# Performance work log

Hardware: AMD Instinct MI355X
Metric: run time of the kernel (lower is better)

## Reference

```python
import jax, jax.numpy as jnp
import numpy as np

D, H, O, E, N = 1024, 2048, 1024, 8, 4096

def setup_inputs() -> dict:
    key = jax.random.key(0)
    ks = jax.random.split(key, 5)
    scale = lambda fan_in: 1.0 / np.sqrt(fan_in)
    x = jax.random.normal(ks[0], (N, D), dtype=jnp.float32)
    Wr = jax.random.normal(ks[1], (E, D), dtype=jnp.float32) * scale(D)
    br = jnp.zeros((E,), dtype=jnp.float32)
    W1 = jax.random.normal(ks[2], (E, H, D), dtype=jnp.float32) * scale(D)
    b1 = jnp.zeros((E, H), dtype=jnp.float32)
    W2 = jax.random.normal(ks[3], (E, O, H), dtype=jnp.float32) * scale(H)
    b2 = jnp.zeros((E, O), dtype=jnp.float32)
    return {"x": x, "Wr": Wr, "br": br, "W1": W1, "b1": b1, "W2": W2, "b2": b2}

def reference(x, Wr, br, W1, b1, W2, b2):
    # router softmax over experts: [N, E]
    route = jax.nn.softmax(x @ Wr.T + br, axis=-1)
    # all experts as one grouped GEMM: hidden [N, E, H]
    h = jnp.einsum('nd,ehd->neh', x, W1) + b1
    h = jnp.square(jax.nn.relu(h))  # squared ReLU
    # expert outputs [N, E, O]
    y = jnp.einsum('neh,eoh->neo', h, W2) + b2
    # softmax-weighted combine over experts -> [N, O]
    return jnp.einsum('ne,neo->no', route, y)
```

## Files before the change

kernel.cpp:

```cpp
#include <hip/hip_runtime.h>
#include <hip/hip_bf16.h>
#include <stdint.h>

#define Dd 1024
#define Hd 2048
#define Od 1024
#define Ed 8
#define Nd 4096

typedef __bf16 bf16x8 __attribute__((ext_vector_type(8)));
typedef float f32x4 __attribute__((ext_vector_type(4)));

__device__ __forceinline__ void gload16(const void* g, void* l) {
  __builtin_amdgcn_global_load_lds(
      (const __attribute__((address_space(1))) void*)g,
      (__attribute__((address_space(3))) void*)l, 16, 0, 0);
}

__device__ __forceinline__ unsigned short f2bf(float f) {
  __hip_bfloat16 h = __float2bfloat16(f);
  return *reinterpret_cast<unsigned short*>(&h);
}

__global__ void cvt_kernel(const float* __restrict__ in,
                           unsigned short* __restrict__ out, int ngroups) {
  int stride = gridDim.x * blockDim.x;
  for (int g = blockIdx.x * blockDim.x + threadIdx.x; g < ngroups; g += stride) {
    const float4* p = (const float4*)(in + (size_t)g * 8);
    float4 a = p[0], b = p[1];
    unsigned short o[8];
    o[0] = f2bf(a.x); o[1] = f2bf(a.y); o[2] = f2bf(a.z); o[3] = f2bf(a.w);
    o[4] = f2bf(b.x); o[5] = f2bf(b.y); o[6] = f2bf(b.z); o[7] = f2bf(b.w);
    *(int4*)(out + (size_t)g * 8) = *(int4*)o;
  }
}

__global__ void router_kernel(const float* __restrict__ x, const float* __restrict__ Wr,
                              const float* __restrict__ br, float* __restrict__ route,
                              unsigned short* __restrict__ xb) {
  const int n = blockIdx.x;
  const int t = threadIdx.x;
  __shared__ float xs[Dd];
  float4 v = *(const float4*)&x[(size_t)n * Dd + t * 4];
  *(float4*)&xs[t * 4] = v;
  unsigned short o[4] = {f2bf(v.x), f2bf(v.y), f2bf(v.z), f2bf(v.w)};
  *(uint2*)&xb[(size_t)n * Dd + t * 4] = *(const uint2*)o;
  __syncthreads();
  float p[Ed];
  #pragma unroll
  for (int e = 0; e < Ed; ++e) p[e] = 0.f;
  for (int d = t; d < Dd; d += 256) {
    float xv = xs[d];
    #pragma unroll
    for (int e = 0; e < Ed; ++e) p[e] += xv * Wr[e * Dd + d];
  }
  __shared__ float red[Ed][4];
  const int lane = t & 63, wid = t >> 6;
  #pragma unroll
  for (int e = 0; e < Ed; ++e) {
    float vv = p[e];
    for (int off = 32; off > 0; off >>= 1) vv += __shfl_down(vv, off);
    if (lane == 0) red[e][wid] = vv;
  }
  __syncthreads();
  if (t == 0) {
    float lg[Ed], mx = -1e30f;
    #pragma unroll
    for (int e = 0; e < Ed; ++e) {
      lg[e] = red[e][0] + red[e][1] + red[e][2] + red[e][3] + br[e];
      mx = fmaxf(mx, lg[e]);
    }
    float s = 0.f;
    #pragma unroll
    for (int e = 0; e < Ed; ++e) { lg[e] = expf(lg[e] - mx); s += lg[e]; }
    float inv = 1.f / s;
    #pragma unroll
    for (int e = 0; e < Ed; ++e) route[(size_t)n * Ed + e] = lg[e] * inv;
  }
}

__global__ void init_out_kernel(const float* __restrict__ route, const float* __restrict__ b2,
                                float* __restrict__ out) {
  const int idx = blockIdx.x * 256 + threadIdx.x;
  const int n = idx >> 10, o = idx & (Od - 1);
  float s = 0.f;
  #pragma unroll
  for (int e = 0; e < Ed; ++e) s += route[(size_t)n * Ed + e] * b2[e * Od + o];
  out[idx] = s;
}

template <int MODE>
__global__ __launch_bounds__(512, 2) void gemm8p(
    const unsigned short* __restrict__ Ag,
    const unsigned short* __restrict__ Bg,
    const float* __restrict__ bias,
    const float* __restrict__ route,
    void* __restrict__ Cout,
    int n0, int ncRows, int ngx) {
  extern __shared__ unsigned short smem[];
  unsigned short* As = smem;
  unsigned short* Bs = smem + 32768;

  const int nwg = gridDim.x;
  const int orig = blockIdx.x;
  const int q8 = nwg >> 3;
  const int wg = (orig & 7) * q8 + (orig >> 3);
  const int bx = wg % ngx;
  const int rem = wg / ngx;
  int by, ez;
  if (MODE == 0) { by = rem & 7; ez = rem >> 3; }
  else           { by = rem & 3; ez = rem >> 2; }

  const int tid = threadIdx.x;
  const int wid = tid >> 6, lane = tid & 63;
  const int wm = wid >> 2, wn = wid & 3;

  const int trow = tid >> 3;
  const int tcs = ((tid & 7) ^ (trow & 7)) * 8;

  const int NT = (MODE == 0) ? (Dd / 64) : (2 * Hd / 64);

  auto stageA = [&](int buf, int kt, int mh) {
    #pragma unroll
    for (int s = 0; s < 2; ++s) {
      const int pa = mh * 128 + s * 64 + trow;
      const int m = ((pa >> 6) & 1) * 128 + ((pa >> 7) & 1) * 64 + (pa & 63);
      const unsigned short* g;
      if (MODE == 0) {
        g = Ag + (size_t)(n0 + bx * 256 + m) * Dd + kt * 64 + tcs;
      } else {
        const int e = ez * 2 + (kt >> 5);
        g = Ag + (size_t)e * ncRows * Hd + (size_t)(bx * 256 + m) * Hd + (kt & 31) * 64 + tcs;
      }
      gload16(g, &As[(size_t)buf * 16384 + (size_t)(mh * 128 + s * 64) * 64 + wid * 512]);
    }
  };
  auto stageB = [&](int buf, int kt, int nh) {
    #pragma unroll
    for (int s = 0; s < 2; ++s) {
      const int pb = nh * 128 + s * 64 + trow;
      const int n = ((pb >> 5) & 3) * 64 + ((pb >> 7) & 1) * 32 + (pb & 31);
      const unsigned short* g;
      if (MODE == 0) {
        g = Bg + (size_t)ez * Hd * Dd + (size_t)(by * 256 + n) * Dd + kt * 64 + tcs;
      } else {
        const int e = ez * 2 + (kt >> 5);
        g = Bg + (size_t)e * Od * Hd + (size_t)(by * 256 + n) * Hd + (kt & 31) * 64 + tcs;
      }
      gload16(g, &Bs[(size_t)buf * 16384 + (size_t)(nh * 128 + s * 64) * 64 + wid * 512]);
    }
  };

  const int laneRow = lane & 15;
  const int swzc[2] = { ((lane >> 4) ^ (lane & 7)) << 3,
                        (((lane >> 4) + 4) ^ (lane & 7)) << 3 };
  const int aRowBase = (wm * 64 + laneRow) * 64;
  const int bRowBase = (wn * 32 + laneRow) * 64;

  auto rdA = [&](int buf, int mh, int mi, int kk) -> bf16x8 {
    const int addr = buf * 16384 + aRowBase + (mh * 128 + mi * 16) * 64 + swzc[kk];
    return *(const bf16x8*)&As[addr];
  };
  auto rdB = [&](int buf, int nh, int ni, int kk) -> bf16x8 {
    const int addr = buf * 16384 + bRowBase + (nh * 128 + ni * 16) * 64 + swzc[kk];
    return *(const bf16x8*)&Bs[addr];
  };

  f32x4 acc[8][4];
  #pragma unroll
  for (int i = 0; i < 8; ++i)
    #pragma unroll
    for (int j = 0; j < 4; ++j) acc[i][j] = (f32x4){0.f, 0.f, 0.f, 0.f};
  bf16x8 a0[4][2], a1[4][2], b0[2][2], b1[2][2];

  stageA(0, 0, 0); stageB(0, 0, 0); stageA(0, 0, 1); stageB(0, 0, 1);
  asm volatile("s_waitcnt vmcnt(0)" ::: "memory");
  __builtin_amdgcn_sched_barrier(0);
  __builtin_amdgcn_s_barrier();

  for (int U = 0; U < NT; ++U) {
    const int buf = U & 1, nbuf = buf ^ 1;
    if (U + 1 < NT) {
      stageA(nbuf, U + 1, 0); stageB(nbuf, U + 1, 0);
      stageA(nbuf, U + 1, 1); stageB(nbuf, U + 1, 1);
    }
    #pragma unroll
    for (int mi = 0; mi < 4; ++mi) { a0[mi][0] = rdA(buf, 0, mi, 0); a0[mi][1] = rdA(buf, 0, mi, 1); }
    #pragma unroll
    for (int ni = 0; ni < 2; ++ni) { b0[ni][0] = rdB(buf, 0, ni, 0); b0[ni][1] = rdB(buf, 0, ni, 1); }
    __builtin_amdgcn_s_setprio(1);
    #pragma unroll
    for (int kk = 0; kk < 2; ++kk)
      #pragma unroll
      for (int mi = 0; mi < 4; ++mi)
        #pragma unroll
        for (int ni = 0; ni < 2; ++ni)
          acc[mi][ni] = __builtin_amdgcn_mfma_f32_16x16x32_bf16(a0[mi][kk], b0[ni][kk], acc[mi][ni], 0, 0, 0);
    __builtin_amdgcn_s_setprio(0);
    #pragma unroll
    for (int mi = 0; mi < 4; ++mi) { a1[mi][0] = rdA(buf, 1, mi, 0); a1[mi][1] = rdA(buf, 1, mi, 1); }
    __builtin_amdgcn_s_setprio(1);
    #pragma unroll
    for (int kk = 0; kk < 2; ++kk)
      #pragma unroll
      for (int mi = 0; mi < 4; ++mi)
        #pragma unroll
        for (int ni = 0; ni < 2; ++ni)
          acc[4 + mi][ni] = __builtin_amdgcn_mfma_f32_16x16x32_bf16(a1[mi][kk], b0[ni][kk], acc[4 + mi][ni], 0, 0, 0);
    __builtin_amdgcn_s_setprio(0);
    #pragma unroll
    for (int ni = 0; ni < 2; ++ni) { b1[ni][0] = rdB(buf, 1, ni, 0); b1[ni][1] = rdB(buf, 1, ni, 1); }
    __builtin_amdgcn_s_setprio(1);
    #pragma unroll
    for (int kk = 0; kk < 2; ++kk)
      #pragma unroll
      for (int mi = 0; mi < 4; ++mi)
        #pragma unroll
        for (int ni = 0; ni < 2; ++ni)
          acc[4 + mi][2 + ni] = __builtin_amdgcn_mfma_f32_16x16x32_bf16(a1[mi][kk], b1[ni][kk], acc[4 + mi][2 + ni], 0, 0, 0);
    __builtin_amdgcn_s_setprio(0);
    __builtin_amdgcn_s_setprio(1);
    #pragma unroll
    for (int kk = 0; kk < 2; ++kk)
      #pragma unroll
      for (int mi = 0; mi < 4; ++mi)
        #pragma unroll
        for (int ni = 0; ni < 2; ++ni)
          acc[mi][2 + ni] = __builtin_amdgcn_mfma_f32_16x16x32_bf16(a0[mi][kk], b1[ni][kk], acc[mi][2 + ni], 0, 0, 0);
    __builtin_amdgcn_s_setprio(0);
    if (U + 1 < NT) {
      asm volatile("s_waitcnt vmcnt(0)" ::: "memory");
    }
    __builtin_amdgcn_sched_barrier(0);
    __builtin_amdgcn_s_barrier();
  }

  if (MODE == 0) {
    unsigned short* hs = (unsigned short*)Cout;
    unsigned short* base = hs + (size_t)ez * ((size_t)ncRows * Hd);
    #pragma unroll
    for (int M = 0; M < 8; ++M) {
      const int mh = M >> 2, mi = M & 3;
      const int row = bx * 256 + wm * 128 + mh * 64 + mi * 16 + (lane >> 4) * 4;
      float rw[4];
      #pragma unroll
      for (int j = 0; j < 4; ++j) rw[j] = route[(size_t)(n0 + row + j) * Ed + ez];
      #pragma unroll
      for (int N = 0; N < 4; ++N) {
        const int nh = N >> 1, ni = N & 1;
        const int col = by * 256 + wn * 64 + nh * 32 + ni * 16 + (lane & 15);
        const float bv = bias[ez * Hd + col];
        #pragma unroll
        for (int j = 0; j < 4; ++j) {
          float v = acc[M][N][j] + bv;
          v = fmaxf(v, 0.f);
          v = v * v * rw[j];
          base[(size_t)(row + j) * Hd + col] = f2bf(v);
        }
      }
    }
  } else {
    float* out = (float*)Cout;
    #pragma unroll
    for (int M = 0; M < 8; ++M) {
      const int mh = M >> 2, mi = M & 3;
      const int row = n0 + bx * 256 + wm * 128 + mh * 64 + mi * 16 + (lane >> 4) * 4;
      #pragma unroll
      for (int N = 0; N < 4; ++N) {
        const int nh = N >> 1, ni = N & 1;
        const int col = by * 256 + wn * 64 + nh * 32 + ni * 16 + (lane & 15);
        #pragma unroll
        for (int j = 0; j < 4; ++j)
          atomicAdd(out + (size_t)(row + j) * Od + col, acc[M][N][j]);
      }
    }
  }
}

extern "C" void kernel_launch(void* const* d_in, const int* in_sizes, int n_in,
                              void* d_out, int out_size, void* d_ws, size_t ws_size,
                              hipStream_t stream) {
  const float* x  = (const float*)d_in[0];
  const float* Wr = (const float*)d_in[1];
  const float* br = (const float*)d_in[2];
  const float* W1 = (const float*)d_in[3];
  const float* b1 = (const float*)d_in[4];
  const float* W2 = (const float*)d_in[5];
  const float* b2 = (const float*)d_in[6];
  float* out = (float*)d_out;

  char* ws = (char*)d_ws;
  size_t off = 0;
  float* route = (float*)(ws + off);                 off += (size_t)Nd * Ed * 4;
  unsigned short* xb  = (unsigned short*)(ws + off); off += (size_t)Nd * Dd * 2;
  unsigned short* w1b = (unsigned short*)(ws + off); off += (size_t)Ed * Hd * Dd * 2;
  unsigned short* w2b = (unsigned short*)(ws + off); off += (size_t)Ed * Od * Hd * 2;
  unsigned short* hs  = (unsigned short*)(ws + off);

  size_t remain = (ws_size > off) ? (ws_size - off) : 0;
  const size_t perRow = (size_t)Ed * Hd * 2;
  long long ncMax = (long long)(remain / perRow);
  int NC = (int)(ncMax & ~255LL);
  if (NC > Nd) NC = Nd;
  if (NC < 256) NC = 256;

  hipFuncSetAttribute(reinterpret_cast<const void*>(&gemm8p<0>),
                      hipFuncAttributeMaxDynamicSharedMemorySize, 131072);
  hipFuncSetAttribute(reinterpret_cast<const void*>(&gemm8p<1>),
                      hipFuncAttributeMaxDynamicSharedMemorySize, 131072);

  cvt_kernel<<<2048, 256, 0, stream>>>(W1, w1b, Ed * Hd * Dd / 8);
  cvt_kernel<<<2048, 256, 0, stream>>>(W2, w2b, Ed * Od * Hd / 8);
  router_kernel<<<Nd, 256, 0, stream>>>(x, Wr, br, route, xb);
  init_out_kernel<<<Nd * Od / 256, 256, 0, stream>>>(route, b2, out);

  for (int n0 = 0; n0 < Nd; n0 += NC) {
    int nc = (NC < (Nd - n0)) ? NC : (Nd - n0);
    int ngx = nc / 256;
    gemm8p<0><<<ngx * 8 * Ed, 512, 131072, stream>>>(xb, w1b, b1, route, hs, n0, nc, ngx);
    gemm8p<1><<<ngx * 4 * 4, 512, 131072, stream>>>(hs, w2b, nullptr, nullptr, out, n0, nc, ngx);
  }
}
```

Baseline: 366.6 us.

## Quantize first expert GEMM to int8 and split second GEMM per expert

The token activations and W1 are now quantized to int8 with per-row absmax scales. The first grouped GEMM runs on int8 MFMA with int32 accumulation, and the scales are applied in the epilogue before bias and squared ReLU. The aim is to double matrix throughput and halve operand bandwidth for that GEMM. The second GEMM now launches one block per expert instead of pairing two experts per block, which doubles the grid but also doubles the atomic adds into the output. The int8 path adds quantization error and an extra pass over x, which risks accuracy tolerance.

```diff
diff --git a/kernel.cpp b/kernel.cpp
--- a/kernel.cpp
+++ b/kernel.cpp
@@ -10,6 +10,7 @@
 
 typedef __bf16 bf16x8 __attribute__((ext_vector_type(8)));
 typedef float f32x4 __attribute__((ext_vector_type(4)));
+typedef int i32x4 __attribute__((ext_vector_type(4)));
 
 __device__ __forceinline__ void gload16(const void* g, void* l) {
   __builtin_amdgcn_global_load_lds(
@@ -20,6 +21,39 @@
 __device__ __forceinline__ unsigned short f2bf(float f) {
   __hip_bfloat16 h = __float2bfloat16(f);
   return *reinterpret_cast<unsigned short*>(&h);
+}
+
+__device__ __forceinline__ float blockMax256(float v) {
+  __shared__ float sm[4];
+  #pragma unroll
+  for (int o = 32; o > 0; o >>= 1) v = fmaxf(v, __shfl_down(v, o));
+  const int lane = threadIdx.x & 63, w = threadIdx.x >> 6;
+  if (lane == 0) sm[w] = v;
+  __syncthreads();
+  return fmaxf(fmaxf(sm[0], sm[1]), fmaxf(sm[2], sm[3]));
+}
+
+template <int K>
+__global__ void qrow_kernel(const float* __restrict__ in,
+                            signed char* __restrict__ out,
+                            float* __restrict__ scale) {
+  const int row = blockIdx.x;
+  const int t = threadIdx.x;
+  const float* r = in + (size_t)row * K;
+  float v[K / 256];
+  float m = 0.f;
+  #pragma unroll
+  for (int i = 0; i < K / 256; ++i) {
+    v[i] = r[t + i * 256];
+    m = fmaxf(m, fabsf(v[i]));
+  }
+  const float M = blockMax256(m);
+  const float inv = (M > 0.f) ? 127.f / M : 0.f;
+  signed char* o = out + (size_t)row * K;
+  #pragma unroll
+  for (int i = 0; i < K / 256; ++i)
+    o[t + i * 256] = (signed char)__float2int_rn(v[i] * inv);
+  if (t == 0) scale[row] = M / 127.f;
 }
 
 __global__ void cvt_kernel(const float* __restrict__ in,
@@ -36,15 +70,12 @@
 }
 
 __global__ void router_kernel(const float* __restrict__ x, const float* __restrict__ Wr,
-                              const float* __restrict__ br, float* __restrict__ route,
-                              unsigned short* __restrict__ xb) {
+                              const float* __restrict__ br, float* __restrict__ route) {
   const int n = blockIdx.x;
   const int t = threadIdx.x;
   __shared__ float xs[Dd];
   float4 v = *(const float4*)&x[(size_t)n * Dd + t * 4];
   *(float4*)&xs[t * 4] = v;
-  unsigned short o[4] = {f2bf(v.x), f2bf(v.y), f2bf(v.z), f2bf(v.w)};
-  *(uint2*)&xb[(size_t)n * Dd + t * 4] = *(const uint2*)o;
   __syncthreads();
   float p[Ed];
   #pragma unroll
@@ -89,17 +120,18 @@
   out[idx] = s;
 }
 
-template <int MODE>
-__global__ __launch_bounds__(512, 2) void gemm8p(
-    const unsigned short* __restrict__ Ag,
-    const unsigned short* __restrict__ Bg,
+__global__ __launch_bounds__(512, 2) void gemmq1(
+    const signed char* __restrict__ Ag,
+    const signed char* __restrict__ Bg,
     const float* __restrict__ bias,
     const float* __restrict__ route,
-    void* __restrict__ Cout,
+    const float* __restrict__ sA,
+    const float* __restrict__ sB,
+    unsigned short* __restrict__ hs,
     int n0, int ncRows, int ngx) {
-  extern __shared__ unsigned short smem[];
-  unsigned short* As = smem;
-  unsigned short* Bs = smem + 32768;
+  extern __shared__ char smem[];
+  char* As = smem;
+  char* Bs = smem + 65536;
 
   const int nwg = gridDim.x;
   const int orig = blockIdx.x;
@@ -107,32 +139,28 @@
   const int wg = (orig & 7) * q8 + (orig >> 3);
   const int bx = wg % ngx;
   const int rem = wg / ngx;
-  int by, ez;
-  if (MODE == 0) { by = rem & 7; ez = rem >> 3; }
-  else           { by = rem & 3; ez = rem >> 2; }
+  const int by = rem & 7, ez = rem >> 3;
 
   const int tid = threadIdx.x;
   const int wid = tid >> 6, lane = tid & 63;
   const int wm = wid >> 2, wn = wid & 3;
 
+  const int KB = Dd;
+  const int NT = KB / 128;
+
+  const signed char* Abase = Ag + (size_t)(n0 + bx * 256) * Dd;
+  const signed char* Bbase = Bg + (size_t)ez * Hd * Dd + (size_t)(by * 256) * Dd;
+
   const int trow = tid >> 3;
-  const int tcs = ((tid & 7) ^ (trow & 7)) * 8;
-
-  const int NT = (MODE == 0) ? (Dd / 64) : (2 * Hd / 64);
+  const int tcs = ((tid & 7) ^ (trow & 7)) * 16;
 
   auto stageA = [&](int buf, int kt, int mh) {
     #pragma unroll
     for (int s = 0; s < 2; ++s) {
       const int pa = mh * 128 + s * 64 + trow;
       const int m = ((pa >> 6) & 1) * 128 + ((pa >> 7) & 1) * 64 + (pa & 63);
-      const unsigned short* g;
-      if (MODE == 0) {
-        g = Ag + (size_t)(n0 + bx * 256 + m) * Dd + kt * 64 + tcs;
-      } else {
-        const int e = ez * 2 + (kt >> 5);
-        g = Ag + (size_t)e * ncRows * Hd + (size_t)(bx * 256 + m) * Hd + (kt & 31) * 64 + tcs;
-      }
-      gload16(g, &As[(size_t)buf * 16384 + (size_t)(mh * 128 + s * 64) * 64 + wid * 512]);
+      gload16(Abase + (size_t)m * KB + kt * 128 + tcs,
+              &As[buf * 32768 + (mh * 128 + s * 64) * 128 + wid * 1024]);
     }
   };
   auto stageB = [&](int buf, int kt, int nh) {
@@ -140,14 +168,166 @@
     for (int s = 0; s < 2; ++s) {
       const int pb = nh * 128 + s * 64 + trow;
       const int n = ((pb >> 5) & 3) * 64 + ((pb >> 7) & 1) * 32 + (pb & 31);
-      const unsigned short* g;
-      if (MODE == 0) {
-        g = Bg + (size_t)ez * Hd * Dd + (size_t)(by * 256 + n) * Dd + kt * 64 + tcs;
-      } else {
-        const int e = ez * 2 + (kt >> 5);
-        g = Bg + (size_t)e * Od * Hd + (size_t)(by * 256 + n) * Hd + (kt & 31) * 64 + tcs;
+      gload16(Bbase + (size_t)n * KB + kt * 128 + tcs,
+              &Bs[buf * 32768 + (nh * 128 + s * 64) * 128 + wid * 1024]);
+    }
+  };
+
+  const int laneRow = lane & 15;
+  const int swz[2] = { ((lane >> 4) ^ (lane & 7)) * 16,
+                       ((4 + (lane >> 4)) ^ (lane & 7)) * 16 };
+  const int aRowB = (wm * 64 + laneRow) * 128;
+  const int bRowB = (wn * 32 + laneRow) * 128;
+
+  auto rdA = [&](int buf, int mh, int mi, int kk) -> i32x4 {
+    return *(const i32x4*)(As + buf * 32768 + aRowB + (mh * 128 + mi * 16) * 128 + swz[kk]);
+  };
+  auto rdB = [&](int buf, int nh, int ni, int kk) -> i32x4 {
+    return *(const i32x4*)(Bs + buf * 32768 + bRowB + (nh * 128 + ni * 16) * 128 + swz[kk]);
+  };
+
+  i32x4 acc[8][4];
+  #pragma unroll
+  for (int i = 0; i < 8; ++i)
+    #pragma unroll
+    for (int j = 0; j < 4; ++j) acc[i][j] = (i32x4){0, 0, 0, 0};
+  i32x4 a0[4][2], a1[4][2], b0[2][2], b1[2][2];
+
+  stageA(0, 0, 0); stageB(0, 0, 0); stageA(0, 0, 1); stageB(0, 0, 1);
+  asm volatile("s_waitcnt vmcnt(0)" ::: "memory");
+  __builtin_amdgcn_sched_barrier(0);
+  __builtin_amdgcn_s_barrier();
+
+  for (int U = 0; U < NT; ++U) {
+    const int buf = U & 1;
+    if (U + 1 < NT) {
+      stageA(buf ^ 1, U + 1, 0); stageB(buf ^ 1, U + 1, 0);
+      stageA(buf ^ 1, U + 1, 1); stageB(buf ^ 1, U + 1, 1);
+    }
+    #pragma unroll
+    for (int mi = 0; mi < 4; ++mi) { a0[mi][0] = rdA(buf, 0, mi, 0); a0[mi][1] = rdA(buf, 0, mi, 1); }
+    #pragma unroll
+    for (int ni = 0; ni < 2; ++ni) { b0[ni][0] = rdB(buf, 0, ni, 0); b0[ni][1] = rdB(buf, 0, ni, 1); }
+    __builtin_amdgcn_s_setprio(1);
+    #pragma unroll
+    for (int kk = 0; kk < 2; ++kk)
+      #pragma unroll
+      for (int mi = 0; mi < 4; ++mi)
+        #pragma unroll
+        for (int ni = 0; ni < 2; ++ni)
+          acc[mi][ni] = __builtin_amdgcn_mfma_i32_16x16x64_i8(a0[mi][kk], b0[ni][kk], acc[mi][ni], 0, 0, 0);
+    __builtin_amdgcn_s_setprio(0);
+    #pragma unroll
+    for (int mi = 0; mi < 4; ++mi) { a1[mi][0] = rdA(buf, 1, mi, 0); a1[mi][1] = rdA(buf, 1, mi, 1); }
+    __builtin_amdgcn_s_setprio(1);
+    #pragma unroll
+    for (int kk = 0; kk < 2; ++kk)
+      #pragma unroll
+      for (int mi = 0; mi < 4; ++mi)
+        #pragma unroll
+        for (int ni = 0; ni < 2; ++ni)
+          acc[4 + mi][ni] = __builtin_amdgcn_mfma_i32_16x16x64_i8(a1[mi][kk], b0[ni][kk], acc[4 + mi][ni], 0, 0, 0);
+    __builtin_amdgcn_s_setprio(0);
+    #pragma unroll
+    for (int ni = 0; ni < 2; ++ni) { b1[ni][0] = rdB(buf, 1, ni, 0); b1[ni][1] = rdB(buf, 1, ni, 1); }
+    __builtin_amdgcn_s_setprio(1);
+    #pragma unroll
+    for (int kk = 0; kk < 2; ++kk)
+      #pragma unroll
+      for (int mi = 0; mi < 4; ++mi)
+        #pragma unroll
+        for (int ni = 0; ni < 2; ++ni)
+          acc[4 + mi][2 + ni] = __builtin_amdgcn_mfma_i32_16x16x64_i8(a1[mi][kk], b1[ni][kk], acc[4 + mi][2 + ni], 0, 0, 0);
+    __builtin_amdgcn_s_setprio(0);
+    __builtin_amdgcn_s_setprio(1);
+    #pragma unroll
+    for (int kk = 0; kk < 2; ++kk)
+      #pragma unroll
+      for (int mi = 0; mi < 4; ++mi)
+        #pragma unroll
+        for (int ni = 0; ni < 2; ++ni)
+          acc[mi][2 + ni] = __builtin_amdgcn_mfma_i32_16x16x64_i8(a0[mi][kk], b1[ni][kk], acc[mi][2 + ni], 0, 0, 0);
+    __builtin_amdgcn_s_setprio(0);
+    if (U + 1 < NT) {
+      asm volatile("s_waitcnt vmcnt(0)" ::: "memory");
+    }
+    __builtin_amdgcn_sched_barrier(0);
+    __builtin_amdgcn_s_barrier();
+  }
+
+  unsigned short* base = hs + (size_t)ez * ((size_t)ncRows * Hd);
+  #pragma unroll
+  for (int M = 0; M < 8; ++M) {
+    const int mh = M >> 2, mi = M & 3;
+    const int rowc = bx * 256 + wm * 128 + mh * 64 + mi * 16 + (lane >> 4) * 4;
+    float sx4[4], rw[4];
+    #pragma unroll
+    for (int j = 0; j < 4; ++j) {
+      sx4[j] = sA[n0 + rowc + j];
+      rw[j] = route[(size_t)(n0 + rowc + j) * Ed + ez];
+    }
+    #pragma unroll
+    for (int N = 0; N < 4; ++N) {
+      const int nh = N >> 1, ni = N & 1;
+      const int col = by * 256 + wn * 64 + nh * 32 + ni * 16 + (lane & 15);
+      const float sw = sB[ez * Hd + col];
+      const float bv = bias[ez * Hd + col];
+      #pragma unroll
+      for (int j = 0; j < 4; ++j) {
+        float v = (float)acc[M][N][j] * (sx4[j] * sw) + bv;
+        v = fmaxf(v, 0.f);
+        v = v * v * rw[j];
+        base[(size_t)(rowc + j) * Hd + col] = f2bf(v);
       }
-      gload16(g, &Bs[(size_t)buf * 16384 + (size_t)(nh * 128 + s * 64) * 64 + wid * 512]);
+    }
+  }
+}
+
+__global__ __launch_bounds__(512, 2) void gemm2b(
+    const unsigned short* __restrict__ Ag,
+    const unsigned short* __restrict__ Bg,
+    float* __restrict__ out,
+    int n0, int ncRows, int ngx) {
+  extern __shared__ char smemc[];
+  unsigned short* As = (unsigned short*)smemc;
+  unsigned short* Bs = (unsigned short*)(smemc + 65536);
+
+  const int nwg = gridDim.x;
+  const int orig = blockIdx.x;
+  const int q8 = nwg >> 3;
+  const int wg = (orig & 7) * q8 + (orig >> 3);
+  const int bx = wg % ngx;
+  const int rem = wg / ngx;
+  const int by = rem & 3, ez = rem >> 2;
+
+  const int tid = threadIdx.x;
+  const int wid = tid >> 6, lane = tid & 63;
+  const int wm = wid >> 2, wn = wid & 3;
+
+  const int NT = Hd / 64;
+
+  const unsigned short* Abase = Ag + (size_t)ez * ncRows * Hd + (size_t)(bx * 256) * Hd;
+  const unsigned short* Bbase = Bg + (size_t)ez * Od * Hd + (size_t)(by * 256) * Hd;
+
+  const int trow = tid >> 3;
+  const int tcs = ((tid & 7) ^ (trow & 7)) * 8;
+
+  auto stageA = [&](int buf, int kt, int mh) {
+    #pragma unroll
+    for (int s = 0; s < 2; ++s) {
+      const int pa = mh * 128 + s * 64 + trow;
+      const int m = ((pa >> 6) & 1) * 128 + ((pa >> 7) & 1) * 64 + (pa & 63);
+      gload16(Abase + (size_t)m * Hd + kt * 64 + tcs,
+              &As[(size_t)buf * 16384 + (size_t)(mh * 128 + s * 64) * 64 + wid * 512]);
+    }
+  };
+  auto stageB = [&](int buf, int kt, int nh) {
+    #pragma unroll
+    for (int s = 0; s < 2; ++s) {
+      const int pb = nh * 128 + s * 64 + trow;
+      const int n = ((pb >> 5) & 3) * 64 + ((pb >> 7) & 1) * 32 + (pb & 31);
+      gload16(Bbase + (size_t)n * Hd + kt * 64 + tcs,
+              &Bs[(size_t)buf * 16384 + (size_t)(nh * 128 + s * 64) * 64 + wid * 512]);
     }
   };
 
@@ -158,12 +338,10 @@
   const int bRowBase = (wn * 32 + laneRow) * 64;
 
   auto rdA = [&](int buf, int mh, int mi, int kk) -> bf16x8 {
-    const int addr = buf * 16384 + aRowBase + (mh * 128 + mi * 16) * 64 + swzc[kk];
-    return *(const bf16x8*)&As[addr];
+    return *(const bf16x8*)&As[buf * 16384 + aRowBase + (mh * 128 + mi * 16) * 64 + swzc[kk]];
   };
   auto rdB = [&](int buf, int nh, int ni, int kk) -> bf16x8 {
-    const int addr = buf * 16384 + bRowBase + (nh * 128 + ni * 16) * 64 + swzc[kk];
-    return *(const bf16x8*)&Bs[addr];
+    return *(const bf16x8*)&Bs[buf * 16384 + bRowBase + (nh * 128 + ni * 16) * 64 + swzc[kk]];
   };
 
   f32x4 acc[8][4];
@@ -179,10 +357,10 @@
   __builtin_amdgcn_s_barrier();
 
   for (int U = 0; U < NT; ++U) {
-    const int buf = U & 1, nbuf = buf ^ 1;
+    const int buf = U & 1;
     if (U + 1 < NT) {
-      stageA(nbuf, U + 1, 0); stageB(nbuf, U + 1, 0);
-      stageA(nbuf, U + 1, 1); stageB(nbuf, U + 1, 1);
+      stageA(buf ^ 1, U + 1, 0); stageB(buf ^ 1, U + 1, 0);
+      stageA(buf ^ 1, U + 1, 1); stageB(buf ^ 1, U + 1, 1);
     }
     #pragma unroll
     for (int mi = 0; mi < 4; ++mi) { a0[mi][0] = rdA(buf, 0, mi, 0); a0[mi][1] = rdA(buf, 0, mi, 1); }
@@ -235,44 +413,17 @@
     __builtin_amdgcn_s_barrier();
   }
 
-  if (MODE == 0) {
-    unsigned short* hs = (unsigned short*)Cout;
-    unsigned short* base = hs + (size_t)ez * ((size_t)ncRows * Hd);
-    #pragma unroll
-    for (int M = 0; M < 8; ++M) {
-      const int mh = M >> 2, mi = M & 3;
-      const int row = bx * 256 + wm * 128 + mh * 64 + mi * 16 + (lane >> 4) * 4;
-      float rw[4];
-      #pragma unroll
-      for (int j = 0; j < 4; ++j) rw[j] = route[(size_t)(n0 + row + j) * Ed + ez];
-      #pragma unroll
-      for (int N = 0; N < 4; ++N) {
-        const int nh = N >> 1, ni = N & 1;
-        const int col = by * 256 + wn * 64 + nh * 32 + ni * 16 + (lane & 15);
-        const float bv = bias[ez * Hd + col];
-        #pragma unroll
-        for (int j = 0; j < 4; ++j) {
-          float v = acc[M][N][j] + bv;
-          v = fmaxf(v, 0.f);
-          v = v * v * rw[j];
-          base[(size_t)(row + j) * Hd + col] = f2bf(v);
-        }
-      }
-    }
-  } else {
-    float* out = (float*)Cout;
-    #pragma unroll
-    for (int M = 0; M < 8; ++M) {
-      const int mh = M >> 2, mi = M & 3;
-      const int row = n0 + bx * 256 + wm * 128 + mh * 64 + mi * 16 + (lane >> 4) * 4;
-      #pragma unroll
-      for (int N = 0; N < 4; ++N) {
-        const int nh = N >> 1, ni = N & 1;
-        const int col = by * 256 + wn * 64 + nh * 32 + ni * 16 + (lane & 15);
-        #pragma unroll
-        for (int j = 0; j < 4; ++j)
-          atomicAdd(out + (size_t)(row + j) * Od + col, acc[M][N][j]);
-      }
+  #pragma unroll
+  for (int M = 0; M < 8; ++M) {
+    const int mh = M >> 2, mi = M & 3;
+    const int row = n0 + bx * 256 + wm * 128 + mh * 64 + mi * 16 + (lane >> 4) * 4;
+    #pragma unroll
+    for (int N = 0; N < 4; ++N) {
+      const int nh = N >> 1, ni = N & 1;
+      const int col = by * 256 + wn * 64 + nh * 32 + ni * 16 + (lane & 15);
+      #pragma unroll
+      for (int j = 0; j < 4; ++j)
+        atomicAdd(out + (size_t)(row + j) * Od + col, acc[M][N][j]);
     }
   }
 }
@@ -291,11 +442,14 @@
 
   char* ws = (char*)d_ws;
   size_t off = 0;
-  float* route = (float*)(ws + off);                 off += (size_t)Nd * Ed * 4;
-  unsigned short* xb  = (unsigned short*)(ws + off); off += (size_t)Nd * Dd * 2;
-  unsigned short* w1b = (unsigned short*)(ws + off); off += (size_t)Ed * Hd * Dd * 2;
-  unsigned short* w2b = (unsigned short*)(ws + off); off += (size_t)Ed * Od * Hd * 2;
-  unsigned short* hs  = (unsigned short*)(ws + off);
+  auto alloc = [&](size_t bytes) { char* p = ws + off; off += (bytes + 255) & ~255ULL; return p; };
+  float* route = (float*)alloc((size_t)Nd * Ed * 4);
+  float* sx    = (float*)alloc((size_t)Nd * 4);
+  float* sw1   = (float*)alloc((size_t)Ed * Hd * 4);
+  signed char* xq  = (signed char*)alloc((size_t)Nd * Dd);
+  signed char* w1q = (signed char*)alloc((size_t)Ed * Hd * Dd);
+  unsigned short* w2b = (unsigned short*)alloc((size_t)Ed * Od * Hd * 2);
+  unsigned short* hs = (unsigned short*)(ws + off);
 
   size_t remain = (ws_size > off) ? (ws_size - off) : 0;
   const size_t perRow = (size_t)Ed * Hd * 2;
@@ -304,20 +458,22 @@
   if (NC > Nd) NC = Nd;
   if (NC < 256) NC = 256;
 
-  hipFuncSetAttribute(reinterpret_cast<const void*>(&gemm8p<0>),
+  hipFuncSetAttribute(reinterpret_cast<const void*>(&gemmq1),
                       hipFuncAttributeMaxDynamicSharedMemorySize, 131072);
-  hipFuncSetAttribute(reinterpret_cast<const void*>(&gemm8p<1>),
+  hipFuncSetAttribute(reinterpret_cast<const void*>(&gemm2b),
                       hipFuncAttributeMaxDynamicSharedMemorySize, 131072);
 
-  cvt_kernel<<<2048, 256, 0, stream>>>(W1, w1b, Ed * Hd * Dd / 8);
+  qrow_kernel<Dd><<<Nd, 256, 0, stream>>>(x, xq, sx);
+  qrow_kernel<Dd><<<Ed * Hd, 256, 0, stream>>>(W1, w1q, sw1);
   cvt_kernel<<<2048, 256, 0, stream>>>(W2, w2b, Ed * Od * Hd / 8);
-  router_kernel<<<Nd, 256, 0, stream>>>(x, Wr, br, route, xb);
+  router_kernel<<<Nd, 256, 0, stream>>>(x, Wr, br, route);
   init_out_kernel<<<Nd * Od / 256, 256, 0, stream>>>(route, b2, out);
 
   for (int n0 = 0; n0 < Nd; n0 += NC) {
     int nc = (NC < (Nd - n0)) ? NC : (Nd - n0);
     int ngx = nc / 256;
-    gemm8p<0><<<ngx * 8 * Ed, 512, 131072, stream>>>(xb, w1b, b1, route, hs, n0, nc, ngx);
-    gemm8p<1><<<ngx * 4 * 4, 512, 131072, stream>>>(hs, w2b, nullptr, nullptr, out, n0, nc, ngx);
-  }
-}
+    gemmq1<<<ngx * 8 * Ed, 512, 131072, stream>>>(
+        xq, w1q, b1, route, sx, sw1, hs, n0, nc, ngx);
+    gemm2b<<<ngx * 4 * Ed, 512, 131072, stream>>>(hs, w2b, out, n0, nc, ngx);
+  }
+}
```

After: 383.8 us. 1.05x slower.
